# Performance work log

Hardware: AMD Instinct MI355X
Metric: run time of the kernel (lower is better)

## Reference

```python
import jax, jax.numpy as jnp
import numpy as np

DIM = 1024
HEADS = 16
HEAD_DIM = DIM // HEADS


def setup_inputs() -> dict:
    key = jax.random.key(0)
    k_x, k_qkv, k_ow, k_ob = jax.random.split(key, 4)
    x = jax.random.normal(k_x, (2, 2048, DIM), dtype=jnp.float32)
    # nn.Linear(dim, 3*dim, bias=False): weight shape [3*dim, dim], y = x @ W.T
    w_qkv = jax.random.normal(k_qkv, (3 * DIM, DIM), dtype=jnp.float32) * (DIM ** -0.5)
    # nn.Linear(dim, dim) with bias
    w_o = jax.random.normal(k_ow, (DIM, DIM), dtype=jnp.float32) * (DIM ** -0.5)
    b_o = jax.random.normal(k_ob, (DIM,), dtype=jnp.float32) * 0.02
    return {"x": x, "w_qkv": w_qkv, "w_o": w_o, "b_o": b_o}


def reference(x, w_qkv, w_o, b_o):
    b, n, _ = x.shape
    scale = DIM ** -0.5  # NOTE: source scales by full dim, not head dim
    # qkv projection: [b, n, 3*dim]
    qkv = jnp.einsum('bnd,ed->bne', x, w_qkv)
    # 'b n (qkv h d) -> qkv b h n d'
    qkv = qkv.reshape(b, n, 3, HEADS, HEAD_DIM)
    q = jnp.transpose(qkv[:, :, 0], (0, 2, 1, 3))  # [b, h, n, d]
    k = jnp.transpose(qkv[:, :, 1], (0, 2, 1, 3))
    v = jnp.transpose(qkv[:, :, 2], (0, 2, 1, 3))
    scores = jnp.einsum('bhqd,bhkd->bhqk', q, k) * scale  # [b, h, n, n]
    attn = jax.nn.softmax(scores, axis=-1)
    out = jnp.einsum('bhqk,bhkd->bhqd', attn, v)  # [b, h, n, d]
    out = jnp.transpose(out, (0, 2, 1, 3)).reshape(b, n, DIM)  # 'b h n d -> b n (h d)'
    out = jnp.einsum('bnd,ed->bne', out, w_o) + b_o
    return out
```

## Files before the change

kernel.cpp:

```cpp
#include <hip/hip_runtime.h>
#include <stdint.h>


#define DIM 1024
#define SEQ 2048
#define BATCH 2
#define ROWS 4096
#define RSTRIDE 3072

typedef __bf16 bf16_t;
typedef bf16_t bf16x4 __attribute__((ext_vector_type(4)));
typedef bf16_t bf16x8 __attribute__((ext_vector_type(8)));
typedef float f32x4 __attribute__((ext_vector_type(4)));

__device__ __forceinline__ ushort f2bf(float f) {
    uint32_t u;
    __builtin_memcpy(&u, &f, 4);
    uint32_t r = (u + 0x7fffu + ((u >> 16) & 1u)) >> 16;
    return (ushort)r;
}

__device__ __forceinline__ void store_out(ushort* p, float v) { *p = f2bf(v); }
__device__ __forceinline__ void store_out(float* p, float v) { *p = v; }

__device__ __forceinline__ void gl_lds16(const void* g, void* l) {
    __builtin_amdgcn_global_load_lds(
        (const __attribute__((address_space(1))) void*)g,
        (__attribute__((address_space(3))) void*)l, 16, 0, 0);
}

__global__ __launch_bounds__(256) void cvt_kernel(
    const float* __restrict__ src, ushort* __restrict__ dst) {
    int i = (blockIdx.x * 256 + threadIdx.x) * 8;
    float4 a = *(const float4*)(src + i);
    float4 b = *(const float4*)(src + i + 4);
    uint4 u;
    u.x = (uint)f2bf(a.x) | ((uint)f2bf(a.y) << 16);
    u.y = (uint)f2bf(a.z) | ((uint)f2bf(a.w) << 16);
    u.z = (uint)f2bf(b.x) | ((uint)f2bf(b.y) << 16);
    u.w = (uint)f2bf(b.z) | ((uint)f2bf(b.w) << 16);
    *(uint4*)(dst + i) = u;
}

template <typename OutT>
__global__ __launch_bounds__(256) void gemm_bt_kernel(
    const ushort* __restrict__ A, const ushort* __restrict__ B,
    const float* __restrict__ bias, OutT* __restrict__ C,
    int M, int N, int K) {
    __shared__ __align__(16) ushort sA[128 * 64];
    __shared__ __align__(16) ushort sB[128 * 64];

    const int tid = threadIdx.x;
    const int lane = tid & 63, w = tid >> 6;
    const int quad = lane >> 4, l15 = lane & 15;
    const int wm = (w >> 1) * 64, wn = (w & 1) * 64;
    const int bm = blockIdx.y, bn = blockIdx.x;

    f32x4 acc[4][4];
#pragma unroll
    for (int i = 0; i < 4; i++)
#pragma unroll
        for (int j = 0; j < 4; j++) acc[i][j] = (f32x4){0.f, 0.f, 0.f, 0.f};

    const ushort* Abase = A + (size_t)(bm * 128) * K;
    const ushort* Bbase = B + (size_t)(bn * 128) * K;
    const int rd = lane >> 3, c8 = lane & 7;
    const int sw = l15 & 7;

    for (int kk = 0; kk < K; kk += 64) {
        __syncthreads();
#pragma unroll
        for (int t = 0; t < 4; t++) {
            int row = w * 32 + t * 8;
            gl_lds16(Abase + (size_t)(row + rd) * K + kk + ((c8 ^ rd) * 8),
                     sA + row * 64);
            gl_lds16(Bbase + (size_t)(row + rd) * K + kk + ((c8 ^ rd) * 8),
                     sB + row * 64);
        }
        __syncthreads();

#pragma unroll
        for (int kh = 0; kh < 2; kh++) {
            bf16x8 af[4], bfr[4];
#pragma unroll
            for (int i = 0; i < 4; i++)
                af[i] = *(const bf16x8*)((const bf16_t*)sA +
                        (wm + i * 16 + l15) * 64 + (((kh * 4 + quad) ^ sw) * 8));
#pragma unroll
            for (int j = 0; j < 4; j++)
                bfr[j] = *(const bf16x8*)((const bf16_t*)sB +
                        (wn + j * 16 + l15) * 64 + (((kh * 4 + quad) ^ sw) * 8));
#pragma unroll
            for (int i = 0; i < 4; i++)
#pragma unroll
                for (int j = 0; j < 4; j++)
                    acc[i][j] = __builtin_amdgcn_mfma_f32_16x16x32_bf16(
                        af[i], bfr[j], acc[i][j], 0, 0, 0);
        }
    }

#pragma unroll
    for (int i = 0; i < 4; i++)
#pragma unroll
        for (int j = 0; j < 4; j++) {
            int col = bn * 128 + wn + j * 16 + l15;
            float bv = bias ? bias[col] : 0.f;
#pragma unroll
            for (int r = 0; r < 4; r++) {
                int row = bm * 128 + wm + i * 16 + quad * 4 + r;
                store_out(&C[(size_t)row * N + col], acc[i][j][r] + bv);
            }
        }
}

__global__ __launch_bounds__(512) void flash_attn_kernel(
    const ushort* __restrict__ qkv, ushort* __restrict__ out) {
    __shared__ __align__(16) ushort sK[128 * 64];
    __shared__ __align__(16) ushort sVt[64 * 128];
    __shared__ __align__(16) ushort sP[128 * 64];

    const int tid = threadIdx.x;
    const int lane = tid & 63, w = tid >> 6;
    const int quad = lane >> 4, l15 = lane & 15;
    const int sw = l15 & 7;
    const int bh = blockIdx.y, b = bh >> 4, h = bh & 15;
    const int q0 = blockIdx.x * 128;
    const ushort* qkvb = qkv + (size_t)b * SEQ * RSTRIDE + h * 64;

    const ushort* qrow = qkvb + (size_t)(q0 + w * 16 + l15) * RSTRIDE;
    const bf16x8 aq0 = *(const bf16x8*)(qrow + quad * 8);
    const bf16x8 aq1 = *(const bf16x8*)(qrow + 32 + quad * 8);

    const int krow = tid >> 3, kc8 = tid & 7;
    const int kdst = krow * 64 + ((kc8 ^ (krow & 7)) * 8);
    const int vrp = tid & 63, vc = tid >> 6;
    const int vch = vrp >> 2, vlo = vrp & 3;

    uint4 kreg0, kreg1, va, vb;
    {
        const ushort* kp0 = qkvb + (size_t)krow * RSTRIDE + DIM + kc8 * 8;
        kreg0 = *(const uint4*)kp0;
        kreg1 = *(const uint4*)(kp0 + (size_t)64 * RSTRIDE);
        const ushort* v0 = qkvb + (size_t)(2 * vrp) * RSTRIDE + 2 * DIM + vc * 8;
        va = *(const uint4*)v0;
        vb = *(const uint4*)(v0 + RSTRIDE);
    }

    f32x4 l_acc = (f32x4){0.f, 0.f, 0.f, 0.f};
    f32x4 o[4];
#pragma unroll
    for (int j = 0; j < 4; j++) o[j] = (f32x4){0.f, 0.f, 0.f, 0.f};

    bf16x8 vones;
#pragma unroll
    for (int e = 0; e < 8; e++) vones[e] = (bf16_t)1.0f;

    const float c_exp = 0.04508422f;

    uint* vt32 = (uint*)sVt;
    bf16_t* sPb = (bf16_t*)sP;
    for (int kb = 0; kb < SEQ; kb += 128) {
        *(uint4*)(sK + kdst) = kreg0;
        *(uint4*)(sK + 64 * 64 + kdst) = kreg1;
        {
            int base = (vc * 8) * 64 + vlo;
            vt32[base + 0 * 64 + ((vch ^ 0) << 2)] = (va.x & 0xffffu) | (vb.x << 16);
            vt32[base + 1 * 64 + ((vch ^ 1) << 2)] = (va.x >> 16) | (vb.x & 0xffff0000u);
            vt32[base + 2 * 64 + ((vch ^ 2) << 2)] = (va.y & 0xffffu) | (vb.y << 16);
            vt32[base + 3 * 64 + ((vch ^ 3) << 2)] = (va.y >> 16) | (vb.y & 0xffff0000u);
            vt32[base + 4 * 64 + ((vch ^ 4) << 2)] = (va.z & 0xffffu) | (vb.z << 16);
            vt32[base + 5 * 64 + ((vch ^ 5) << 2)] = (va.z >> 16) | (vb.z & 0xffff0000u);
            vt32[base + 6 * 64 + ((vch ^ 6) << 2)] = (va.w & 0xffffu) | (vb.w << 16);
            vt32[base + 7 * 64 + ((vch ^ 7) << 2)] = (va.w >> 16) | (vb.w & 0xffff0000u);
        }
        __syncthreads();

        int nkb = (kb + 128 < SEQ) ? kb + 128 : kb;
        {
            const ushort* kp0 = qkvb + (size_t)(nkb + krow) * RSTRIDE + DIM + kc8 * 8;
            kreg0 = *(const uint4*)kp0;
            kreg1 = *(const uint4*)(kp0 + (size_t)64 * RSTRIDE);
            const ushort* v0 =
                qkvb + (size_t)(nkb + 2 * vrp) * RSTRIDE + 2 * DIM + vc * 8;
            va = *(const uint4*)v0;
            vb = *(const uint4*)(v0 + RSTRIDE);
        }

        f32x4 s[8];
#pragma unroll
        for (int j = 0; j < 8; j++) {
            const ushort* kp = sK + (j * 16 + l15) * 64;
            bf16x8 bk0 = *(const bf16x8*)(kp + ((quad ^ sw) * 8));
            bf16x8 bk1 = *(const bf16x8*)(kp + (((4 | quad) ^ sw) * 8));
            f32x4 z = (f32x4){0.f, 0.f, 0.f, 0.f};
            __builtin_amdgcn_s_setprio(1);
            z = __builtin_amdgcn_mfma_f32_16x16x32_bf16(aq0, bk0, z, 0, 0, 0);
            z = __builtin_amdgcn_mfma_f32_16x16x32_bf16(aq1, bk1, z, 0, 0, 0);
            __builtin_amdgcn_s_setprio(0);
            s[j] = z;
        }

#pragma unroll
        for (int h2 = 0; h2 < 2; h2++) {
#pragma unroll
            for (int j = 0; j < 4; j++)
#pragma unroll
                for (int r = 0; r < 4; r++) {
                    float p = __builtin_amdgcn_exp2f(s[h2 * 4 + j][r] * c_exp);
                    int row = w * 16 + quad * 4 + r;
                    int ch = j * 2 + (l15 >> 3);
                    sPb[row * 64 +
                        (((ch ^ ((quad * 4 + r) & 7)) << 3) | (l15 & 7))] =
                        (bf16_t)p;
                }
            const bf16_t* pp = sPb + (w * 16 + l15) * 64;
            bf16x8 pa0 = *(const bf16x8*)(pp + ((quad ^ sw) * 8));
            bf16x8 pa1 = *(const bf16x8*)(pp + (((4 | quad) ^ sw) * 8));
            __builtin_amdgcn_s_setprio(1);
            l_acc = __builtin_amdgcn_mfma_f32_16x16x32_bf16(pa0, vones, l_acc, 0, 0, 0);
            l_acc = __builtin_amdgcn_mfma_f32_16x16x32_bf16(pa1, vones, l_acc, 0, 0, 0);
            __builtin_amdgcn_s_setprio(0);
#pragma unroll
            for (int jd = 0; jd < 4; jd++) {
                const bf16_t* vp = (const bf16_t*)sVt + (jd * 16 + l15) * 128;
                bf16x8 bv0 = *(const bf16x8*)(vp + (((h2 * 8 + quad) ^ sw) * 8));
                bf16x8 bv1 = *(const bf16x8*)(vp + (((h2 * 8 + 4 + quad) ^ sw) * 8));
                __builtin_amdgcn_s_setprio(1);
                o[jd] = __builtin_amdgcn_mfma_f32_16x16x32_bf16(pa0, bv0, o[jd], 0, 0, 0);
                o[jd] = __builtin_amdgcn_mfma_f32_16x16x32_bf16(pa1, bv1, o[jd], 0, 0, 0);
                __builtin_amdgcn_s_setprio(0);
            }
        }
        __syncthreads();
    }

#pragma unroll
    for (int r = 0; r < 4; r++) {
        float inv = 1.f / l_acc[r];
        int qrow_i = q0 + w * 16 + quad * 4 + r;
#pragma unroll
        for (int j = 0; j < 4; j++) {
            out[(size_t)(b * SEQ + qrow_i) * DIM + h * 64 + j * 16 + l15] =
                f2bf(o[j][r] * inv);
        }
    }
}

extern "C" void kernel_launch(void* const* d_in, const int* in_sizes, int n_in,
                              void* d_out, int out_size, void* d_ws, size_t ws_size,
                              hipStream_t stream) {
    const float* x = (const float*)d_in[0];
    const float* w_qkv = (const float*)d_in[1];
    const float* w_o = (const float*)d_in[2];
    const float* b_o = (const float*)d_in[3];
    float* out = (float*)d_out;

    ushort* qkv = (ushort*)d_ws;
    ushort* attn = qkv + (size_t)ROWS * 3 * DIM;
    ushort* xb = attn + (size_t)ROWS * DIM;
    ushort* wqkvb = xb + (size_t)ROWS * DIM;
    ushort* wob = wqkvb + (size_t)3 * DIM * DIM;

    dim3 blk(256);
    cvt_kernel<<<ROWS * DIM / 2048, blk, 0, stream>>>(x, xb);
    cvt_kernel<<<3 * DIM * DIM / 2048, blk, 0, stream>>>(w_qkv, wqkvb);
    cvt_kernel<<<DIM * DIM / 2048, blk, 0, stream>>>(w_o, wob);

    gemm_bt_kernel<ushort><<<dim3(3 * DIM / 128, ROWS / 128), blk, 0, stream>>>(
        xb, wqkvb, nullptr, qkv, ROWS, 3 * DIM, DIM);
    flash_attn_kernel<<<dim3(SEQ / 128, BATCH * 16), dim3(512), 0, stream>>>(qkv, attn);
    gemm_bt_kernel<float><<<dim3(DIM / 128, ROWS / 128), blk, 0, stream>>>(
        attn, wob, b_o, out, ROWS, DIM, DIM);
}
```

Before: 200.2 us.

## Fuse conversion kernels and reorder K/V staging in flash attention loop

Merges the three fp32-to-bf16 conversion launches into one kernel that picks its source by index, removing launch overhead. In the attention loop, the K tile is stored to shared memory at the end of the previous iteration, so the QK MFMAs can start right after the V write. The next-tile global loads are issued after QK, and the sync moves accordingly. This changes how load latency overlaps compute and may expose global load latency differently.

```diff
diff --git a/kernel.cpp b/kernel.cpp
--- a/kernel.cpp
+++ b/kernel.cpp
@@ -29,11 +29,23 @@
         (__attribute__((address_space(3))) void*)l, 16, 0, 0);
 }
 
-__global__ __launch_bounds__(256) void cvt_kernel(
-    const float* __restrict__ src, ushort* __restrict__ dst) {
-    int i = (blockIdx.x * 256 + threadIdx.x) * 8;
-    float4 a = *(const float4*)(src + i);
-    float4 b = *(const float4*)(src + i + 4);
+__global__ __launch_bounds__(256) void cvt3_kernel(
+    const float* __restrict__ x, const float* __restrict__ wq,
+    const float* __restrict__ wo, ushort* __restrict__ dst) {
+    size_t i = ((size_t)blockIdx.x * 256 + threadIdx.x) * 8;
+    const size_t n_x = (size_t)ROWS * DIM;
+    const size_t n_wq = (size_t)3 * DIM * DIM;
+    const float* src;
+    size_t off;
+    if (i < n_x) {
+        src = x; off = i;
+    } else if (i < n_x + n_wq) {
+        src = wq; off = i - n_x;
+    } else {
+        src = wo; off = i - n_x - n_wq;
+    }
+    float4 a = *(const float4*)(src + off);
+    float4 b = *(const float4*)(src + off + 4);
     uint4 u;
     u.x = (uint)f2bf(a.x) | ((uint)f2bf(a.y) << 16);
     u.y = (uint)f2bf(a.z) | ((uint)f2bf(a.w) << 16);
@@ -159,9 +171,12 @@
 
     uint* vt32 = (uint*)sVt;
     bf16_t* sPb = (bf16_t*)sP;
+
+    *(uint4*)(sK + kdst) = kreg0;
+    *(uint4*)(sK + 64 * 64 + kdst) = kreg1;
+    __syncthreads();
+
     for (int kb = 0; kb < SEQ; kb += 128) {
-        *(uint4*)(sK + kdst) = kreg0;
-        *(uint4*)(sK + 64 * 64 + kdst) = kreg1;
         {
             int base = (vc * 8) * 64 + vlo;
             vt32[base + 0 * 64 + ((vch ^ 0) << 2)] = (va.x & 0xffffu) | (vb.x << 16);
@@ -173,18 +188,6 @@
             vt32[base + 6 * 64 + ((vch ^ 6) << 2)] = (va.w & 0xffffu) | (vb.w << 16);
             vt32[base + 7 * 64 + ((vch ^ 7) << 2)] = (va.w >> 16) | (vb.w & 0xffff0000u);
         }
-        __syncthreads();
-
-        int nkb = (kb + 128 < SEQ) ? kb + 128 : kb;
-        {
-            const ushort* kp0 = qkvb + (size_t)(nkb + krow) * RSTRIDE + DIM + kc8 * 8;
-            kreg0 = *(const uint4*)kp0;
-            kreg1 = *(const uint4*)(kp0 + (size_t)64 * RSTRIDE);
-            const ushort* v0 =
-                qkvb + (size_t)(nkb + 2 * vrp) * RSTRIDE + 2 * DIM + vc * 8;
-            va = *(const uint4*)v0;
-            vb = *(const uint4*)(v0 + RSTRIDE);
-        }
 
         f32x4 s[8];
 #pragma unroll
@@ -199,6 +202,18 @@
             __builtin_amdgcn_s_setprio(0);
             s[j] = z;
         }
+
+        int nkb = (kb + 128 < SEQ) ? kb + 128 : kb;
+        {
+            const ushort* kp0 = qkvb + (size_t)(nkb + krow) * RSTRIDE + DIM + kc8 * 8;
+            kreg0 = *(const uint4*)kp0;
+            kreg1 = *(const uint4*)(kp0 + (size_t)64 * RSTRIDE);
+            const ushort* v0 =
+                qkvb + (size_t)(nkb + 2 * vrp) * RSTRIDE + 2 * DIM + vc * 8;
+            va = *(const uint4*)v0;
+            vb = *(const uint4*)(v0 + RSTRIDE);
+        }
+        __syncthreads();
 
 #pragma unroll
         for (int h2 = 0; h2 < 2; h2++) {
@@ -231,6 +246,9 @@
                 __builtin_amdgcn_s_setprio(0);
             }
         }
+
+        *(uint4*)(sK + kdst) = kreg0;
+        *(uint4*)(sK + 64 * 64 + kdst) = kreg1;
         __syncthreads();
     }
 
@@ -262,9 +280,8 @@
     ushort* wob = wqkvb + (size_t)3 * DIM * DIM;
 
     dim3 blk(256);
-    cvt_kernel<<<ROWS * DIM / 2048, blk, 0, stream>>>(x, xb);
-    cvt_kernel<<<3 * DIM * DIM / 2048, blk, 0, stream>>>(w_qkv, wqkvb);
-    cvt_kernel<<<DIM * DIM / 2048, blk, 0, stream>>>(w_o, wob);
+    cvt3_kernel<<<(ROWS * DIM + 3 * DIM * DIM + DIM * DIM) / 2048, blk, 0,
+                  stream>>>(x, w_qkv, w_o, xb);
 
     gemm_bt_kernel<ushort><<<dim3(3 * DIM / 128, ROWS / 128), blk, 0, stream>>>(
         xb, wqkvb, nullptr, qkv, ROWS, 3 * DIM, DIM);
```

New measurement: 202.7 us. About the same (+1.3%).
